# Performance work log

Hardware: AMD Instinct MI355X
Metric: run time of the kernel (lower is better)

## Reference

```python
import jax, jax.numpy as jnp
import numpy as np

B, N, D, H = 2, 2048, 256, 4
DH = D // H  # 64
ALPHA_DIV = 0.01
LN_EPS = 1e-5


def _split_heads(t):
    # [B, N, D] -> [B, H, N, DH]
    b, n, _ = t.shape
    return t.reshape(b, n, H, DH).transpose(0, 2, 1, 3)


def _merge_heads(t):
    # [B, H, N, DH] -> [B, N, D]
    b, h, n, d = t.shape
    return t.transpose(0, 2, 1, 3).reshape(b, n, h * d)


def setup_inputs() -> dict:
    key = jax.random.key(0)
    ks = jax.random.split(key, 20)
    p = lambda k, shape: (jax.random.normal(k, shape, dtype=jnp.float32) * 0.02)
    return {
        "x0": jax.random.normal(ks[0], (B, N, D), dtype=jnp.float32),
        "x1": jax.random.normal(ks[1], (B, N, D), dtype=jnp.float32),
        "cross_mask0": jax.random.uniform(ks[2], (B, 1, N), dtype=jnp.float32),
        "cross_mask1": jax.random.uniform(ks[3], (B, 1, N), dtype=jnp.float32),
        # weights stored as [in, out]
        "Wqk": p(ks[4], (D, D)), "bqk": jnp.zeros((D,), jnp.float32),
        "Wv": p(ks[5], (D, D)), "bv": jnp.zeros((D,), jnp.float32),
        "Wo": p(ks[6], (D, D)), "bo": jnp.zeros((D,), jnp.float32),
        "W1": p(ks[7], (2 * D, 2 * D)), "b1": jnp.zeros((2 * D,), jnp.float32),
        "ln_g": jnp.ones((2 * D,), jnp.float32), "ln_b": jnp.zeros((2 * D,), jnp.float32),
        "W2": p(ks[8], (2 * D, D)), "b2": jnp.zeros((D,), jnp.float32),
    }


def _ffn(x, W1, b1, ln_g, ln_b, W2, b2):
    h = x @ W1 + b1
    mu = jnp.mean(h, -1, keepdims=True)
    var = jnp.var(h, -1, keepdims=True)
    h = (h - mu) * jax.lax.rsqrt(var + LN_EPS) * ln_g + ln_b
    h = jax.nn.gelu(h, approximate=False)
    return h @ W2 + b2


def cross_block(x0, x1, cross_mask0, cross_mask1, Wqk, bqk, Wv, bv, Wo, bo,
                W1, b1, ln_g, ln_b, W2, b2):
    s = (DH ** -0.5) ** 0.5  # scale applied to each of qk0, qk1
    qk0 = _split_heads(x0 @ Wqk + bqk) * s
    qk1 = _split_heads(x1 @ Wqk + bqk) * s
    v0 = _split_heads(x0 @ Wv + bv)
    v1 = _split_heads(x1 @ Wv + bv)

    sim = jnp.einsum('bhid,bhjd->bhij', qk0, qk1)  # [B,H,N0,N1]

    # cross masks: [B,1,N] -> broadcast [B,1,1,N] over heads and query rows
    bad0 = (cross_mask0[:, :, None, :] < ALPHA_DIV)  # masks keys of dir 1->0
    bad1 = (cross_mask1[:, :, None, :] < ALPHA_DIV)  # masks keys of dir 0->1

    attn01 = jax.nn.softmax(jnp.where(bad1, -jnp.inf, sim), axis=-1)             # [B,H,N0,N1]
    attn10 = jax.nn.softmax(jnp.where(bad0, -jnp.inf, sim.swapaxes(-2, -1)), axis=-1)  # [B,H,N1,N0]

    m0 = jnp.einsum('bhij,bhjd->bhid', attn01, v1)
    m1 = jnp.einsum('bhij,bhjd->bhid', attn10, v0)

    m0 = _merge_heads(m0) @ Wo + bo
    m1 = _merge_heads(m1) @ Wo + bo

    out0 = x0 + _ffn(jnp.concatenate([x0, m0], -1), W1, b1, ln_g, ln_b, W2, b2)
    out1 = x1 + _ffn(jnp.concatenate([x1, m1], -1), W1, b1, ln_g, ln_b, W2, b2)
    return out0, out1, attn01, attn10


def reference(x0, x1, cross_mask0, cross_mask1, Wqk, bqk, Wv, bv, Wo, bo,
              W1, b1, ln_g, ln_b, W2, b2):
    return cross_block(x0, x1, cross_mask0, cross_mask1, Wqk, bqk, Wv, bv,
                       Wo, bo, W1, b1, ln_g, ln_b, W2, b2)
```

## Files before the change

kernel.cpp:

```cpp
#include <hip/hip_runtime.h>
#include <hip/hip_bf16.h>
#include <math.h>

#define B 2
#define N 2048
#define D 256
#define H 4
#define DH 64
#define D2 512
#define BH 8
#define BKP 40

static constexpr float ALPHA_DIV = 0.01f;
static constexpr float LN_EPS = 1e-5f;
static constexpr float SCL = 0.35355339059327373f;

typedef __attribute__((ext_vector_type(4))) float f32x4;
typedef __attribute__((ext_vector_type(8))) short s16x8;

template<int BM, bool OUT_BF16, bool HAS_RES>
__device__ __forceinline__ void gemm_core(
    __hip_bfloat16 (*As)[BKP], __hip_bfloat16 (*Ws)[BKP],
    const __hip_bfloat16* A, int lda, const __hip_bfloat16* WT, int ldw,
    const float* bias, const float* Res, int ldres,
    void* Cvp, int ldc, int K, float alpha, int rowBase, int colBase)
{
    constexpr int WM = BM / 2;
    constexpr int FM = WM / 16;
    constexpr int ACHUNK = (BM * 32) / (256 * 8);

    const int tid = threadIdx.x;
    const int lane = tid & 63, wid = tid >> 6;
    const int wr = wid >> 1, wc = wid & 1;
    const int lr = lane & 15, lk = (lane >> 4) * 8;

    f32x4 acc[FM][2] = {};

    for (int k0 = 0; k0 < K; k0 += 32) {
#pragma unroll
        for (int c = 0; c < ACHUNK; c++) {
            int e = (tid + c * 256) * 8;
            int r = e >> 5, kk = e & 31;
            *(s16x8*)&As[r][kk] = *(const s16x8*)&A[(size_t)(rowBase + r) * lda + k0 + kk];
        }
        {
            int e = tid * 8;
            int n = e >> 5, kk = e & 31;
            *(s16x8*)&Ws[n][kk] = *(const s16x8*)&WT[(size_t)(colBase + n) * ldw + k0 + kk];
        }
        __syncthreads();

        s16x8 a[FM], b[2];
#pragma unroll
        for (int i = 0; i < FM; i++) a[i] = *(const s16x8*)&As[wr * WM + i * 16 + lr][lk];
#pragma unroll
        for (int j = 0; j < 2; j++) b[j] = *(const s16x8*)&Ws[wc * 32 + j * 16 + lr][lk];
#pragma unroll
        for (int i = 0; i < FM; i++)
#pragma unroll
            for (int j = 0; j < 2; j++)
                acc[i][j] = __builtin_amdgcn_mfma_f32_16x16x32_bf16(a[i], b[j], acc[i][j], 0, 0, 0);
        __syncthreads();
    }

#pragma unroll
    for (int i = 0; i < FM; i++) {
#pragma unroll
        for (int j = 0; j < 2; j++) {
            int col = colBase + wc * 32 + j * 16 + lr;
            float bval = bias ? bias[col] : 0.f;
#pragma unroll
            for (int t = 0; t < 4; t++) {
                int row = rowBase + wr * WM + i * 16 + (lane >> 4) * 4 + t;
                float o = alpha * (acc[i][j][t] + bval);
                if (HAS_RES) o += Res[(size_t)row * ldres + col];
                if (OUT_BF16)
                    ((__hip_bfloat16*)Cvp)[(size_t)row * ldc + col] = __float2bfloat16(o);
                else
                    ((float*)Cvp)[(size_t)row * ldc + col] = o;
            }
        }
    }
}

template<bool OUT_BF16, bool HAS_RES>
__global__ __launch_bounds__(256) void gemm128_z(
    const __hip_bfloat16* A0, const __hip_bfloat16* A1, int lda,
    const __hip_bfloat16* WT, int ldw, const float* bias,
    const float* Res0, const float* Res1, int ldres,
    void* C0, void* C1, int ldc, int K, float alpha)
{
    __shared__ __hip_bfloat16 As[128][BKP];
    __shared__ __hip_bfloat16 Ws[64][BKP];
    const __hip_bfloat16* A = blockIdx.z ? A1 : A0;
    const float* Res = blockIdx.z ? Res1 : Res0;
    void* C = blockIdx.z ? C1 : C0;
    gemm_core<128, OUT_BF16, HAS_RES>(As, Ws, A, lda, WT, ldw, bias, Res, ldres,
        C, ldc, K, alpha, blockIdx.y * 128, blockIdx.x * 64);
}

__global__ __launch_bounds__(256) void proj_kernel(
    const float* __restrict__ x0, const float* __restrict__ x1,
    const __hip_bfloat16* __restrict__ WcT, const float* __restrict__ cb,
    __hip_bfloat16* __restrict__ qkv0, __hip_bfloat16* __restrict__ qkv1,
    __hip_bfloat16* __restrict__ vT,
    __hip_bfloat16* __restrict__ xc0, __hip_bfloat16* __restrict__ xc1)
{
    __shared__ __hip_bfloat16 As[128][BKP];
    __shared__ __hip_bfloat16 Ws[64][BKP];
    __shared__ __hip_bfloat16 T[128][72];
    const int z = blockIdx.z;
    const float* x = z ? x1 : x0;
    __hip_bfloat16* qkv = z ? qkv1 : qkv0;
    __hip_bfloat16* xc = z ? xc1 : xc0;
    const int rowBase = blockIdx.y * 128;
    const int colBase = blockIdx.x * 64;
    const int tid = threadIdx.x;
    const int lane = tid & 63, wid = tid >> 6;
    const int wr = wid >> 1, wc = wid & 1;
    const int lr = lane & 15, g = lane >> 4, lk = g * 8;

    f32x4 acc[4][2] = {};
    for (int k0 = 0; k0 < D; k0 += 32) {
#pragma unroll
        for (int c = 0; c < 2; c++) {
            int e = (tid + c * 256) * 8;
            int r = e >> 5, kk = e & 31;
            const float4 v0 = *(const float4*)&x[(size_t)(rowBase + r) * D + k0 + kk];
            const float4 v1 = *(const float4*)&x[(size_t)(rowBase + r) * D + k0 + kk + 4];
            union { s16x8 v; __hip_bfloat16 hh[8]; } u;
            u.hh[0] = __float2bfloat16(v0.x); u.hh[1] = __float2bfloat16(v0.y);
            u.hh[2] = __float2bfloat16(v0.z); u.hh[3] = __float2bfloat16(v0.w);
            u.hh[4] = __float2bfloat16(v1.x); u.hh[5] = __float2bfloat16(v1.y);
            u.hh[6] = __float2bfloat16(v1.z); u.hh[7] = __float2bfloat16(v1.w);
            *(s16x8*)&As[r][kk] = u.v;
            if (colBase == 0)
                *(s16x8*)&xc[(size_t)(rowBase + r) * D2 + k0 + kk] = u.v;
        }
        {
            int e = tid * 8;
            int n = e >> 5, kk = e & 31;
            *(s16x8*)&Ws[n][kk] = *(const s16x8*)&WcT[(size_t)(colBase + n) * D + k0 + kk];
        }
        __syncthreads();
        s16x8 a[4], b[2];
#pragma unroll
        for (int i = 0; i < 4; i++) a[i] = *(const s16x8*)&As[wr * 64 + i * 16 + lr][lk];
#pragma unroll
        for (int j = 0; j < 2; j++) b[j] = *(const s16x8*)&Ws[wc * 32 + j * 16 + lr][lk];
#pragma unroll
        for (int i = 0; i < 4; i++)
#pragma unroll
            for (int j = 0; j < 2; j++)
                acc[i][j] = __builtin_amdgcn_mfma_f32_16x16x32_bf16(a[i], b[j], acc[i][j], 0, 0, 0);
        __syncthreads();
    }

    if (colBase < 256) {
#pragma unroll
        for (int i = 0; i < 4; i++)
#pragma unroll
            for (int j = 0; j < 2; j++) {
                int col = colBase + wc * 32 + j * 16 + lr;
                float bval = cb[col];
#pragma unroll
                for (int t = 0; t < 4; t++) {
                    int row = rowBase + wr * 64 + i * 16 + g * 4 + t;
                    qkv[(size_t)row * D2 + col] = __float2bfloat16(acc[i][j][t] + bval);
                }
            }
    } else {
#pragma unroll
        for (int i = 0; i < 4; i++)
#pragma unroll
            for (int j = 0; j < 2; j++) {
                int cl = wc * 32 + j * 16 + lr;
                float bval = cb[colBase + cl];
#pragma unroll
                for (int t = 0; t < 4; t++)
                    T[wr * 64 + i * 16 + g * 4 + t][cl] = __float2bfloat16(acc[i][j][t] + bval);
            }
        __syncthreads();
        int hh = (colBase - 256) >> 6;
        int b_ = rowBase >> 11, n0 = rowBase & (N - 1);
        int slot = (z ? 0 : 8) + b_ * H + hh;
        int dh = tid >> 2, nn0 = (tid & 3) * 32;
        alignas(16) __hip_bfloat16 tmp[32];
#pragma unroll
        for (int u = 0; u < 32; u++) tmp[u] = T[nn0 + u][dh];
        __hip_bfloat16* dst = vT + ((size_t)slot * DH + dh) * N + n0 + nn0;
#pragma unroll
        for (int u8 = 0; u8 < 4; u8++)
            *(s16x8*)&dst[u8 * 8] = *(s16x8*)&tmp[u8 * 8];
    }
}

__device__ void transpose_tile(const float* W, int ldw, __hip_bfloat16* WT, int ldt,
                               int n0, int k0, float scale)
{
    __shared__ float T[32][33];
    int t = threadIdx.x;
    int r = t >> 3, c = (t & 7) * 4;
    float4 v = *(const float4*)&W[(size_t)(k0 + r) * ldw + n0 + c];
    T[r][c] = v.x; T[r][c + 1] = v.y; T[r][c + 2] = v.z; T[r][c + 3] = v.w;
    __syncthreads();
    __hip_bfloat16* dst = &WT[(size_t)(n0 + r) * ldt + k0 + c];
    dst[0] = __float2bfloat16(T[c][r] * scale);
    dst[1] = __float2bfloat16(T[c + 1][r] * scale);
    dst[2] = __float2bfloat16(T[c + 2][r] * scale);
    dst[3] = __float2bfloat16(T[c + 3][r] * scale);
}

__global__ __launch_bounds__(256) void prep_weights(
    const float* Wqk, const float* Wv, const float* W1, const float* W2,
    const float* bqk, const float* bv,
    __hip_bfloat16* WcT, __hip_bfloat16* W1cT, __hip_bfloat16* W2T,
    float* cb)
{
    int blk = blockIdx.x;
    if (blk < 64) {
        int nT = blk & 7, kT = blk >> 3;
        transpose_tile(Wqk, 256, WcT, 256, nT * 32, kT * 32, SCL);
    } else if (blk < 128) {
        int t = blk - 64; int nT = t & 7, kT = t >> 3;
        transpose_tile(Wv, 256, WcT + 256 * 256, 256, nT * 32, kT * 32, 1.f);
    } else if (blk < 256) {
        int t = blk - 128; int nT = t & 15, kT = t >> 4;
        transpose_tile(W1, 512, W1cT, 512, nT * 32, kT * 32, 1.f);
    } else if (blk < 384) {
        int t = blk - 256; int nT = t & 7, kT = t >> 3;
        transpose_tile(W2, 256, W2T, 512, nT * 32, kT * 32, 1.f);
    } else {
        int t = threadIdx.x;
        cb[t] = SCL * bqk[t];
        cb[256 + t] = bv[t];
    }
}

__global__ __launch_bounds__(256) void fuse_w(
    const float* __restrict__ Wo, const float* __restrict__ W1,
    const float* __restrict__ b1, const float* __restrict__ bo,
    __hip_bfloat16* __restrict__ W1cT, float* __restrict__ cb2)
{
    int blk = blockIdx.x;
    if (blk < 32) {
        __shared__ float As[64][17];
        __shared__ float Bs[64][17];
        int n0 = (blk & 7) * 64, k0 = (blk >> 3) * 64;
        int tx = threadIdx.x & 15, ty = threadIdx.x >> 4;
        float acc[4][4] = {};
        for (int c0 = 0; c0 < 256; c0 += 16) {
#pragma unroll
            for (int it = 0; it < 4; it++) {
                int idx = threadIdx.x + it * 256;
                int n = idx & 63, c = idx >> 6;
                As[n][c] = W1[(size_t)(256 + c0 + c) * 512 + n0 + n];
            }
#pragma unroll
            for (int it = 0; it < 4; it++) {
                int idx = threadIdx.x + it * 256;
                int k = idx >> 4, c = idx & 15;
                Bs[k][c] = Wo[(size_t)(k0 + k) * 256 + c0 + c];
            }
            __syncthreads();
#pragma unroll
            for (int c = 0; c < 16; c++) {
                float av[4], bv[4];
#pragma unroll
                for (int i = 0; i < 4; i++) av[i] = As[ty + i * 16][c];
#pragma unroll
                for (int j = 0; j < 4; j++) bv[j] = Bs[tx + j * 16][c];
#pragma unroll
                for (int i = 0; i < 4; i++)
#pragma unroll
                    for (int j = 0; j < 4; j++) acc[i][j] += av[i] * bv[j];
            }
            __syncthreads();
        }
#pragma unroll
        for (int i = 0; i < 4; i++)
#pragma unroll
            for (int j = 0; j < 4; j++)
                W1cT[(size_t)(n0 + ty + i * 16) * 512 + 256 + k0 + tx + j * 16] =
                    __float2bfloat16(acc[i][j]);
    } else {
        int n = (blk - 32) * 256 + threadIdx.x;
        float s = b1[n];
        for (int c = 0; c < 256; c++) s += bo[c] * W1[(size_t)(256 + c) * 512 + n];
        cb2[n] = s;
    }
}

__global__ __launch_bounds__(256) void fused_attn_av(
    const __hip_bfloat16* __restrict__ qkv0, const __hip_bfloat16* __restrict__ qkv1,
    const float* __restrict__ cm0, const float* __restrict__ cm1,
    const __hip_bfloat16* __restrict__ vT,
    float* __restrict__ attn01, float* __restrict__ attn10,
    __hip_bfloat16* __restrict__ xc0, __hip_bfloat16* __restrict__ xc1)
{
    __shared__ __hip_bfloat16 Kt[128][72];
    __shared__ __hip_bfloat16 Pfb[64][136];
    __shared__ float okm[2048];

    const int tid = threadIdx.x;
    int l = blockIdx.x;
    int xcd = l & 7, idx = l >> 3;
    int zz = xcd * 2 + (idx >> 5);
    int xb = idx & 31;
    int dir = zz >> 3, bh = zz & 7;
    int b = bh >> 2, h = bh & 3;

    const __hip_bfloat16* qQ = (dir ? qkv1 : qkv0) + (size_t)b * N * D2 + h * DH;
    const __hip_bfloat16* qK = (dir ? qkv0 : qkv1) + (size_t)b * N * D2 + h * DH;
    const float* cmK = (dir ? cm0 : cm1) + b * N;
    const __hip_bfloat16* vslot = vT + (size_t)((dir ? 8 : 0) + bh) * DH * N;
    float* attnOut = (dir ? attn10 : attn01) + (size_t)bh * N * N;
    __hip_bfloat16* mOut = (dir ? xc1 : xc0) + (size_t)b * N * D2 + 256 + h * DH;

    const int i0 = xb * 64;
    const int lane = tid & 63, w = tid >> 6;
    const int lr = lane & 15, g = lane >> 4;

    s16x8 a0 = *(const s16x8*)&qQ[(size_t)(i0 + w * 16 + lr) * D2 + g * 8];
    s16x8 a1 = *(const s16x8*)&qQ[(size_t)(i0 + w * 16 + lr) * D2 + 32 + g * 8];

#pragma unroll
    for (int it = 0; it < 8; it++) okm[tid + it * 256] = cmK[tid + it * 256];

    s16x8 kreg[4];
    auto loadK = [&](int jt) {
        const int kk0 = jt * 128;
#pragma unroll
        for (int c = 0; c < 4; c++) {
            int e = (tid + c * 256) * 8;
            kreg[c] = *(const s16x8*)&qK[(size_t)(kk0 + (e >> 6)) * D2 + (e & 63)];
        }
    };
    auto writeK = [&]() {
#pragma unroll
        for (int c = 0; c < 4; c++) {
            int e = (tid + c * 256) * 8;
            *(s16x8*)&Kt[e >> 6][e & 63] = kreg[c];
        }
    };

    float sp[4] = { 0.f, 0.f, 0.f, 0.f };
    loadK(0);
    for (int jt = 0; jt < 16; jt++) {
        writeK();
        __syncthreads();
        if (jt < 15) loadK(jt + 1);

        f32x4 accs[8] = {};
#pragma unroll
        for (int j = 0; j < 8; j++) {
            s16x8 bb = *(const s16x8*)&Kt[j * 16 + lr][g * 8];
            accs[j] = __builtin_amdgcn_mfma_f32_16x16x32_bf16(a0, bb, accs[j], 0, 0, 0);
        }
#pragma unroll
        for (int j = 0; j < 8; j++) {
            s16x8 bb = *(const s16x8*)&Kt[j * 16 + lr][32 + g * 8];
            accs[j] = __builtin_amdgcn_mfma_f32_16x16x32_bf16(a1, bb, accs[j], 0, 0, 0);
        }
        const int k0 = jt * 128;
#pragma unroll
        for (int j = 0; j < 8; j++) {
            bool ok = okm[k0 + j * 16 + lr] >= ALPHA_DIV;
#pragma unroll
            for (int t = 0; t < 4; t++)
                if (ok) sp[t] += __expf(accs[j][t]);
        }
        __syncthreads();
    }
    float inv[4];
#pragma unroll
    for (int t = 0; t < 4; t++) {
#pragma unroll
        for (int off = 1; off <= 8; off <<= 1) sp[t] += __shfl_xor(sp[t], off);
        inv[t] = 1.f / sp[t];
    }

    f32x4 acc_o[4] = {};
    loadK(0);
    for (int jt = 0; jt < 16; jt++) {
        writeK();
        __syncthreads();
        if (jt < 15) loadK(jt + 1);
        const int k0 = jt * 128;

        s16x8 vf[4][4];
#pragma unroll
        for (int ks = 0; ks < 4; ks++)
#pragma unroll
            for (int j = 0; j < 4; j++)
                vf[ks][j] = *(const s16x8*)&vslot[(size_t)(j * 16 + lr) * N + k0 + ks * 32 + g * 8];

        f32x4 accs[8] = {};
#pragma unroll
        for (int j = 0; j < 8; j++) {
            s16x8 bb = *(const s16x8*)&Kt[j * 16 + lr][g * 8];
            accs[j] = __builtin_amdgcn_mfma_f32_16x16x32_bf16(a0, bb, accs[j], 0, 0, 0);
        }
#pragma unroll
        for (int j = 0; j < 8; j++) {
            s16x8 bb = *(const s16x8*)&Kt[j * 16 + lr][32 + g * 8];
            accs[j] = __builtin_amdgcn_mfma_f32_16x16x32_bf16(a1, bb, accs[j], 0, 0, 0);
        }

#pragma unroll
        for (int j = 0; j < 8; j++) {
            bool ok = okm[k0 + j * 16 + lr] >= ALPHA_DIV;
#pragma unroll
            for (int t = 0; t < 4; t++) {
                float pv = ok ? __expf(accs[j][t]) * inv[t] : 0.f;
                Pfb[w * 16 + g * 4 + t][j * 16 + lr] = __float2bfloat16(pv);
            }
        }
        __syncthreads();

#pragma unroll
        for (int k = 0; k < 4; k++) {
            int f = tid + k * 256;
            int r = f >> 4, c0 = (f & 15) * 8;
            union { s16x8 v; __hip_bfloat16 hh[8]; } u;
            u.v = *(const s16x8*)&Pfb[r][c0];
            float4 o0, o1;
            o0.x = __bfloat162float(u.hh[0]); o0.y = __bfloat162float(u.hh[1]);
            o0.z = __bfloat162float(u.hh[2]); o0.w = __bfloat162float(u.hh[3]);
            o1.x = __bfloat162float(u.hh[4]); o1.y = __bfloat162float(u.hh[5]);
            o1.z = __bfloat162float(u.hh[6]); o1.w = __bfloat162float(u.hh[7]);
            *(float4*)&attnOut[(size_t)(i0 + r) * N + k0 + c0] = o0;
            *(float4*)&attnOut[(size_t)(i0 + r) * N + k0 + c0 + 4] = o1;
        }

#pragma unroll
        for (int ks = 0; ks < 4; ks++) {
            s16x8 pa = *(const s16x8*)&Pfb[w * 16 + lr][ks * 32 + g * 8];
#pragma unroll
            for (int j = 0; j < 4; j++)
                acc_o[j] = __builtin_amdgcn_mfma_f32_16x16x32_bf16(pa, vf[ks][j], acc_o[j], 0, 0, 0);
        }
        __syncthreads();
    }

    __hip_bfloat16* Ob = (__hip_bfloat16*)Pfb;
#pragma unroll
    for (int j = 0; j < 4; j++)
#pragma unroll
        for (int t = 0; t < 4; t++)
            Ob[(w * 16 + g * 4 + t) * 136 + j * 16 + lr] = __float2bfloat16(acc_o[j][t]);
    __syncthreads();
    {
        int row = tid >> 2, c0 = (tid & 3) * 16;
        *(s16x8*)&mOut[(size_t)(i0 + row) * D2 + c0]     = *(const s16x8*)&Ob[row * 136 + c0];
        *(s16x8*)&mOut[(size_t)(i0 + row) * D2 + c0 + 8] = *(const s16x8*)&Ob[row * 136 + c0 + 8];
    }
}

#define HS_LD 528
__global__ __launch_bounds__(256) void w1_ln_gelu(
    __hip_bfloat16* __restrict__ xc0, __hip_bfloat16* __restrict__ xc1,
    const __hip_bfloat16* __restrict__ W1T, const float* __restrict__ b1,
    const float* __restrict__ lng, const float* __restrict__ lnb)
{
    __shared__ __hip_bfloat16 As[32][BKP];
    __shared__ __hip_bfloat16 WH[512 * BKP];
    __shared__ float redS[4][32], redQ[4][32];

    __hip_bfloat16* xc = blockIdx.y ? xc1 : xc0;
    const int rowBase = blockIdx.x * 32;
    const int tid = threadIdx.x;
    const int w = tid >> 6, lane = tid & 63;
    const int lr = lane & 15, g = lane >> 4, lk = g * 8;

    f32x4 acc[2][8] = {};
    for (int k0 = 0; k0 < D2; k0 += 32) {
        if (tid < 128) {
            int e = tid * 8;
            int r = e >> 5, kk = e & 31;
            *(s16x8*)&As[r][kk] = *(const s16x8*)&xc[(size_t)(rowBase + r) * D2 + k0 + kk];
        }
#pragma unroll
        for (int c = 0; c < 8; c++) {
            int e = (tid + c * 256) * 8;
            int n = e >> 5, kk = e & 31;
            *(s16x8*)&WH[n * BKP + kk] = *(const s16x8*)&W1T[(size_t)n * D2 + k0 + kk];
        }
        __syncthreads();
        s16x8 a[2], b[8];
#pragma unroll
        for (int i = 0; i < 2; i++) a[i] = *(const s16x8*)&As[i * 16 + lr][lk];
#pragma unroll
        for (int j = 0; j < 8; j++) b[j] = *(const s16x8*)&WH[(w * 128 + j * 16 + lr) * BKP + lk];
#pragma unroll
        for (int i = 0; i < 2; i++)
#pragma unroll
            for (int j = 0; j < 8; j++)
                acc[i][j] = __builtin_amdgcn_mfma_f32_16x16x32_bf16(a[i], b[j], acc[i][j], 0, 0, 0);
        __syncthreads();
    }

    float cols_b[8];
#pragma unroll
    for (int j = 0; j < 8; j++) cols_b[j] = b1[w * 128 + j * 16 + lr];
#pragma unroll
    for (int i = 0; i < 2; i++) {
#pragma unroll
        for (int t = 0; t < 4; t++) {
            float s = 0.f, q = 0.f;
#pragma unroll
            for (int j = 0; j < 8; j++) {
                float hv = acc[i][j][t] + cols_b[j];
                acc[i][j][t] = hv;
                s += hv; q += hv * hv;
            }
#pragma unroll
            for (int off = 1; off <= 8; off <<= 1) {
                s += __shfl_xor(s, off);
                q += __shfl_xor(q, off);
            }
            if (lr == 0) {
                int row = i * 16 + g * 4 + t;
                redS[w][row] = s; redQ[w][row] = q;
            }
        }
    }
    __syncthreads();

    __hip_bfloat16* Hs = WH;
    float gcol[8], bcol[8];
#pragma unroll
    for (int j = 0; j < 8; j++) {
        gcol[j] = lng[w * 128 + j * 16 + lr];
        bcol[j] = lnb[w * 128 + j * 16 + lr];
    }
#pragma unroll
    for (int i = 0; i < 2; i++) {
#pragma unroll
        for (int t = 0; t < 4; t++) {
            int row = i * 16 + g * 4 + t;
            float sum = redS[0][row] + redS[1][row] + redS[2][row] + redS[3][row];
            float sq  = redQ[0][row] + redQ[1][row] + redQ[2][row] + redQ[3][row];
            float mu = sum * (1.f / 512.f);
            float var = sq * (1.f / 512.f) - mu * mu;
            float rstd = rsqrtf(var + LN_EPS);
#pragma unroll
            for (int j = 0; j < 8; j++) {
                float y = (acc[i][j][t] - mu) * rstd * gcol[j] + bcol[j];
                float ge = 0.5f * y * (1.f + erff(y * 0.70710678118654752f));
                Hs[row * HS_LD + w * 128 + j * 16 + lr] = __float2bfloat16(ge);
            }
        }
    }
    __syncthreads();

    {
        int row = tid >> 3, c0 = (tid & 7) * 64;
#pragma unroll
        for (int u = 0; u < 8; u++)
            *(s16x8*)&xc[(size_t)(rowBase + row) * D2 + c0 + u * 8] =
                *(s16x8*)&Hs[row * HS_LD + c0 + u * 8];
    }
}

extern "C" void kernel_launch(void* const* d_in, const int* in_sizes, int n_in,
                              void* d_out, int out_size, void* d_ws, size_t ws_size,
                              hipStream_t stream) {
    const float* x0  = (const float*)d_in[0];
    const float* x1  = (const float*)d_in[1];
    const float* cm0 = (const float*)d_in[2];
    const float* cm1 = (const float*)d_in[3];
    const float* Wqk = (const float*)d_in[4]; const float* bqk = (const float*)d_in[5];
    const float* Wv  = (const float*)d_in[6]; const float* bv  = (const float*)d_in[7];
    const float* Wo  = (const float*)d_in[8]; const float* bo  = (const float*)d_in[9];
    const float* W1  = (const float*)d_in[10]; const float* b1 = (const float*)d_in[11];
    const float* lng = (const float*)d_in[12]; const float* lnb = (const float*)d_in[13];
    const float* W2  = (const float*)d_in[14]; const float* b2 = (const float*)d_in[15];

    float* out = (float*)d_out;
    char* p = (char*)d_ws;

    const size_t XSZ = (size_t)B * N * D;
    auto alloc = [&](size_t bytes) { char* r = p; p += (bytes + 255) & ~255ull; return r; };
    __hip_bfloat16* qkv0 = (__hip_bfloat16*)alloc((size_t)B * N * D2 * 2);
    __hip_bfloat16* qkv1 = (__hip_bfloat16*)alloc((size_t)B * N * D2 * 2);
    __hip_bfloat16* vT   = (__hip_bfloat16*)alloc((size_t)16 * DH * N * 2);
    __hip_bfloat16* xc0  = (__hip_bfloat16*)alloc((size_t)B * N * D2 * 2);
    __hip_bfloat16* xc1  = (__hip_bfloat16*)alloc((size_t)B * N * D2 * 2);
    __hip_bfloat16* WcT  = (__hip_bfloat16*)alloc(512 * 256 * 2);
    __hip_bfloat16* W1cT = (__hip_bfloat16*)alloc(512 * 512 * 2);
    __hip_bfloat16* W2T  = (__hip_bfloat16*)alloc(256 * 512 * 2);
    float* cb            = (float*)alloc(512 * 4);
    float* cb2           = (float*)alloc(512 * 4);

    float* out0 = out;
    float* out1 = out + XSZ;
    float* attn01 = out + 2 * XSZ;
    float* attn10 = attn01 + (size_t)BH * N * N;

    dim3 blk(256);

    prep_weights<<<385, blk, 0, stream>>>(Wqk, Wv, W1, W2, bqk, bv,
                                          WcT, W1cT, W2T, cb);
    fuse_w<<<34, blk, 0, stream>>>(Wo, W1, b1, bo, W1cT, cb2);

    proj_kernel<<<dim3(8, 32, 2), blk, 0, stream>>>(
        x0, x1, WcT, cb, qkv0, qkv1, vT, xc0, xc1);

    fused_attn_av<<<512, blk, 0, stream>>>(qkv0, qkv1, cm0, cm1, vT,
        attn01, attn10, xc0, xc1);

    w1_ln_gelu<<<dim3(128, 2), blk, 0, stream>>>(xc0, xc1, W1cT, cb2, lng, lnb);

    gemm128_z<false, true><<<dim3(4, 32, 2), blk, 0, stream>>>(
        xc0, xc1, D2, W2T, D2, b2, x0, x1, D, out0, out1, D, D2, 1.f);
}
```

Measured before the change: 205.0 us.

## Halve query tile and split key columns across wave pairs in attention kernel

The fused attention kernel now processes 32 query rows per block instead of 64, launching 1024 blocks. Within a block, pairs of waves split each 128-key tile into two 64-column halves, reducing softmax denominators and partial PV outputs through shared memory. It also drops one barrier per tile, loads V fragments inline instead of prefetching into registers, and adds occupancy launch bounds. The aim is more parallelism and occupancy across CUs, at the cost of reloading K tiles twice as often overall and extra reduction overhead.

```diff
diff --git a/kernel.cpp b/kernel.cpp
--- a/kernel.cpp
+++ b/kernel.cpp
@@ -291,7 +291,7 @@
     }
 }
 
-__global__ __launch_bounds__(256) void fused_attn_av(
+__global__ __launch_bounds__(256, 4) void fused_attn_av(
     const __hip_bfloat16* __restrict__ qkv0, const __hip_bfloat16* __restrict__ qkv1,
     const float* __restrict__ cm0, const float* __restrict__ cm1,
     const __hip_bfloat16* __restrict__ vT,
@@ -299,14 +299,15 @@
     __hip_bfloat16* __restrict__ xc0, __hip_bfloat16* __restrict__ xc1)
 {
     __shared__ __hip_bfloat16 Kt[128][72];
-    __shared__ __hip_bfloat16 Pfb[64][136];
+    __shared__ __hip_bfloat16 Pfb[32][144];
     __shared__ float okm[2048];
+    __shared__ float redS[4][16];
 
     const int tid = threadIdx.x;
     int l = blockIdx.x;
     int xcd = l & 7, idx = l >> 3;
-    int zz = xcd * 2 + (idx >> 5);
-    int xb = idx & 31;
+    int zz = xcd * 2 + (idx >> 6);
+    int xb = idx & 63;
     int dir = zz >> 3, bh = zz & 7;
     int b = bh >> 2, h = bh & 3;
 
@@ -317,12 +318,14 @@
     float* attnOut = (dir ? attn10 : attn01) + (size_t)bh * N * N;
     __hip_bfloat16* mOut = (dir ? xc1 : xc0) + (size_t)b * N * D2 + 256 + h * DH;
 
-    const int i0 = xb * 64;
+    const int i0 = xb * 32;
     const int lane = tid & 63, w = tid >> 6;
+    const int f = w >> 1, hf = w & 1;
+    const int kb = hf * 64;
     const int lr = lane & 15, g = lane >> 4;
 
-    s16x8 a0 = *(const s16x8*)&qQ[(size_t)(i0 + w * 16 + lr) * D2 + g * 8];
-    s16x8 a1 = *(const s16x8*)&qQ[(size_t)(i0 + w * 16 + lr) * D2 + 32 + g * 8];
+    s16x8 a0 = *(const s16x8*)&qQ[(size_t)(i0 + f * 16 + lr) * D2 + g * 8];
+    s16x8 a1 = *(const s16x8*)&qQ[(size_t)(i0 + f * 16 + lr) * D2 + 32 + g * 8];
 
 #pragma unroll
     for (int it = 0; it < 8; it++) okm[tid + it * 256] = cmK[tid + it * 256];
@@ -351,34 +354,41 @@
         __syncthreads();
         if (jt < 15) loadK(jt + 1);
 
-        f32x4 accs[8] = {};
-#pragma unroll
-        for (int j = 0; j < 8; j++) {
-            s16x8 bb = *(const s16x8*)&Kt[j * 16 + lr][g * 8];
+        f32x4 accs[4] = {};
+#pragma unroll
+        for (int j = 0; j < 4; j++) {
+            s16x8 bb = *(const s16x8*)&Kt[kb + j * 16 + lr][g * 8];
             accs[j] = __builtin_amdgcn_mfma_f32_16x16x32_bf16(a0, bb, accs[j], 0, 0, 0);
         }
 #pragma unroll
-        for (int j = 0; j < 8; j++) {
-            s16x8 bb = *(const s16x8*)&Kt[j * 16 + lr][32 + g * 8];
+        for (int j = 0; j < 4; j++) {
+            s16x8 bb = *(const s16x8*)&Kt[kb + j * 16 + lr][32 + g * 8];
             accs[j] = __builtin_amdgcn_mfma_f32_16x16x32_bf16(a1, bb, accs[j], 0, 0, 0);
         }
         const int k0 = jt * 128;
 #pragma unroll
-        for (int j = 0; j < 8; j++) {
-            bool ok = okm[k0 + j * 16 + lr] >= ALPHA_DIV;
+        for (int j = 0; j < 4; j++) {
+            bool ok = okm[k0 + kb + j * 16 + lr] >= ALPHA_DIV;
 #pragma unroll
             for (int t = 0; t < 4; t++)
                 if (ok) sp[t] += __expf(accs[j][t]);
         }
         __syncthreads();
     }
+#pragma unroll
+    for (int t = 0; t < 4; t++) {
+#pragma unroll
+        for (int off = 1; off <= 8; off <<= 1) sp[t] += __shfl_xor(sp[t], off);
+    }
+    if (lr == 0) {
+#pragma unroll
+        for (int t = 0; t < 4; t++) redS[w][g * 4 + t] = sp[t];
+    }
+    __syncthreads();
     float inv[4];
 #pragma unroll
-    for (int t = 0; t < 4; t++) {
-#pragma unroll
-        for (int off = 1; off <= 8; off <<= 1) sp[t] += __shfl_xor(sp[t], off);
-        inv[t] = 1.f / sp[t];
-    }
+    for (int t = 0; t < 4; t++)
+        inv[t] = 1.f / (redS[f * 2][g * 4 + t] + redS[f * 2 + 1][g * 4 + t]);
 
     f32x4 acc_o[4] = {};
     loadK(0);
@@ -388,72 +398,79 @@
         if (jt < 15) loadK(jt + 1);
         const int k0 = jt * 128;
 
-        s16x8 vf[4][4];
-#pragma unroll
-        for (int ks = 0; ks < 4; ks++)
-#pragma unroll
-            for (int j = 0; j < 4; j++)
-                vf[ks][j] = *(const s16x8*)&vslot[(size_t)(j * 16 + lr) * N + k0 + ks * 32 + g * 8];
-
-        f32x4 accs[8] = {};
-#pragma unroll
-        for (int j = 0; j < 8; j++) {
-            s16x8 bb = *(const s16x8*)&Kt[j * 16 + lr][g * 8];
+        f32x4 accs[4] = {};
+#pragma unroll
+        for (int j = 0; j < 4; j++) {
+            s16x8 bb = *(const s16x8*)&Kt[kb + j * 16 + lr][g * 8];
             accs[j] = __builtin_amdgcn_mfma_f32_16x16x32_bf16(a0, bb, accs[j], 0, 0, 0);
         }
 #pragma unroll
-        for (int j = 0; j < 8; j++) {
-            s16x8 bb = *(const s16x8*)&Kt[j * 16 + lr][32 + g * 8];
+        for (int j = 0; j < 4; j++) {
+            s16x8 bb = *(const s16x8*)&Kt[kb + j * 16 + lr][32 + g * 8];
             accs[j] = __builtin_amdgcn_mfma_f32_16x16x32_bf16(a1, bb, accs[j], 0, 0, 0);
         }
 
 #pragma unroll
-        for (int j = 0; j < 8; j++) {
-            bool ok = okm[k0 + j * 16 + lr] >= ALPHA_DIV;
+        for (int j = 0; j < 4; j++) {
+            bool ok = okm[k0 + kb + j * 16 + lr] >= ALPHA_DIV;
 #pragma unroll
             for (int t = 0; t < 4; t++) {
                 float pv = ok ? __expf(accs[j][t]) * inv[t] : 0.f;
-                Pfb[w * 16 + g * 4 + t][j * 16 + lr] = __float2bfloat16(pv);
-            }
-        }
-        __syncthreads();
-
-#pragma unroll
-        for (int k = 0; k < 4; k++) {
-            int f = tid + k * 256;
-            int r = f >> 4, c0 = (f & 15) * 8;
+                Pfb[f * 16 + g * 4 + t][kb + j * 16 + lr] = __float2bfloat16(pv);
+            }
+        }
+
+        {
+            int r = f * 16 + (lane >> 2), cs = kb + (lane & 3) * 16;
             union { s16x8 v; __hip_bfloat16 hh[8]; } u;
-            u.v = *(const s16x8*)&Pfb[r][c0];
-            float4 o0, o1;
-            o0.x = __bfloat162float(u.hh[0]); o0.y = __bfloat162float(u.hh[1]);
-            o0.z = __bfloat162float(u.hh[2]); o0.w = __bfloat162float(u.hh[3]);
-            o1.x = __bfloat162float(u.hh[4]); o1.y = __bfloat162float(u.hh[5]);
-            o1.z = __bfloat162float(u.hh[6]); o1.w = __bfloat162float(u.hh[7]);
-            *(float4*)&attnOut[(size_t)(i0 + r) * N + k0 + c0] = o0;
-            *(float4*)&attnOut[(size_t)(i0 + r) * N + k0 + c0 + 4] = o1;
-        }
-
-#pragma unroll
-        for (int ks = 0; ks < 4; ks++) {
-            s16x8 pa = *(const s16x8*)&Pfb[w * 16 + lr][ks * 32 + g * 8];
-#pragma unroll
-            for (int j = 0; j < 4; j++)
-                acc_o[j] = __builtin_amdgcn_mfma_f32_16x16x32_bf16(pa, vf[ks][j], acc_o[j], 0, 0, 0);
-        }
-        __syncthreads();
-    }
-
-    __hip_bfloat16* Ob = (__hip_bfloat16*)Pfb;
-#pragma unroll
-    for (int j = 0; j < 4; j++)
-#pragma unroll
-        for (int t = 0; t < 4; t++)
-            Ob[(w * 16 + g * 4 + t) * 136 + j * 16 + lr] = __float2bfloat16(acc_o[j][t]);
+#pragma unroll
+            for (int half = 0; half < 2; half++) {
+                u.v = *(const s16x8*)&Pfb[r][cs + half * 8];
+                float4 o;
+                o.x = __bfloat162float(u.hh[0]); o.y = __bfloat162float(u.hh[1]);
+                o.z = __bfloat162float(u.hh[2]); o.w = __bfloat162float(u.hh[3]);
+                *(float4*)&attnOut[(size_t)(i0 + r) * N + k0 + cs + half * 8] = o;
+                o.x = __bfloat162float(u.hh[4]); o.y = __bfloat162float(u.hh[5]);
+                o.z = __bfloat162float(u.hh[6]); o.w = __bfloat162float(u.hh[7]);
+                *(float4*)&attnOut[(size_t)(i0 + r) * N + k0 + cs + half * 8 + 4] = o;
+            }
+        }
+
+#pragma unroll
+        for (int ks = 0; ks < 2; ks++) {
+            s16x8 pa = *(const s16x8*)&Pfb[f * 16 + lr][kb + ks * 32 + g * 8];
+#pragma unroll
+            for (int j = 0; j < 4; j++) {
+                s16x8 vb = *(const s16x8*)&vslot[(size_t)(j * 16 + lr) * N + k0 + kb + ks * 32 + g * 8];
+                acc_o[j] = __builtin_amdgcn_mfma_f32_16x16x32_bf16(pa, vb, acc_o[j], 0, 0, 0);
+            }
+        }
+        __syncthreads();
+    }
+
+    float (*Of)[72] = (float(*)[72])Pfb;
+    if (hf == 0) {
+#pragma unroll
+        for (int j = 0; j < 4; j++)
+#pragma unroll
+            for (int t = 0; t < 4; t++)
+                Of[f * 16 + g * 4 + t][j * 16 + lr] = acc_o[j][t];
+    }
+    __syncthreads();
+    if (hf == 1) {
+#pragma unroll
+        for (int j = 0; j < 4; j++)
+#pragma unroll
+            for (int t = 0; t < 4; t++)
+                Of[f * 16 + g * 4 + t][j * 16 + lr] += acc_o[j][t];
+    }
     __syncthreads();
     {
-        int row = tid >> 2, c0 = (tid & 3) * 16;
-        *(s16x8*)&mOut[(size_t)(i0 + row) * D2 + c0]     = *(const s16x8*)&Ob[row * 136 + c0];
-        *(s16x8*)&mOut[(size_t)(i0 + row) * D2 + c0 + 8] = *(const s16x8*)&Ob[row * 136 + c0 + 8];
+        int row = tid >> 3, c0 = (tid & 7) * 8;
+        union { s16x8 v; __hip_bfloat16 hh[8]; } u;
+#pragma unroll
+        for (int i = 0; i < 8; i++) u.hh[i] = __float2bfloat16(Of[row][c0 + i]);
+        *(s16x8*)&mOut[(size_t)(i0 + row) * D2 + c0] = u.v;
     }
 }
 
@@ -607,7 +624,7 @@
     proj_kernel<<<dim3(8, 32, 2), blk, 0, stream>>>(
         x0, x1, WcT, cb, qkv0, qkv1, vT, xc0, xc1);
 
-    fused_attn_av<<<512, blk, 0, stream>>>(qkv0, qkv1, cm0, cm1, vT,
+    fused_attn_av<<<1024, blk, 0, stream>>>(qkv0, qkv1, cm0, cm1, vT,
         attn01, attn10, xc0, xc1);
 
     w1_ln_gelu<<<dim3(128, 2), blk, 0, stream>>>(xc0, xc1, W1cT, cb2, lng, lnb);
```

Result: slower. 228.2 us (+11.3%).

## Fuse W2 GEMM into the LN/GELU kernel and merge weight-prep launches

Applied to the files above, without the earlier changes.

The second FFN GEMM, with its bias and residual add, now runs at the end of the W1+LayerNorm+GELU kernel, straight from the GELU activations held in shared memory. This drops the bf16 write-back of the hidden activations, their re-read and one kernel launch. The Wo·W1 weight-folding kernel is also merged into prep_weights as extra blocks, removing another launch. In the fused tail each wave reads W2T fragments directly from global memory without staging them in shared memory, which may add L2 traffic.

```diff
diff --git a/kernel.cpp b/kernel.cpp
--- a/kernel.cpp
+++ b/kernel.cpp
@@ -17,87 +17,6 @@
 
 typedef __attribute__((ext_vector_type(4))) float f32x4;
 typedef __attribute__((ext_vector_type(8))) short s16x8;
-
-template<int BM, bool OUT_BF16, bool HAS_RES>
-__device__ __forceinline__ void gemm_core(
-    __hip_bfloat16 (*As)[BKP], __hip_bfloat16 (*Ws)[BKP],
-    const __hip_bfloat16* A, int lda, const __hip_bfloat16* WT, int ldw,
-    const float* bias, const float* Res, int ldres,
-    void* Cvp, int ldc, int K, float alpha, int rowBase, int colBase)
-{
-    constexpr int WM = BM / 2;
-    constexpr int FM = WM / 16;
-    constexpr int ACHUNK = (BM * 32) / (256 * 8);
-
-    const int tid = threadIdx.x;
-    const int lane = tid & 63, wid = tid >> 6;
-    const int wr = wid >> 1, wc = wid & 1;
-    const int lr = lane & 15, lk = (lane >> 4) * 8;
-
-    f32x4 acc[FM][2] = {};
-
-    for (int k0 = 0; k0 < K; k0 += 32) {
-#pragma unroll
-        for (int c = 0; c < ACHUNK; c++) {
-            int e = (tid + c * 256) * 8;
-            int r = e >> 5, kk = e & 31;
-            *(s16x8*)&As[r][kk] = *(const s16x8*)&A[(size_t)(rowBase + r) * lda + k0 + kk];
-        }
-        {
-            int e = tid * 8;
-            int n = e >> 5, kk = e & 31;
-            *(s16x8*)&Ws[n][kk] = *(const s16x8*)&WT[(size_t)(colBase + n) * ldw + k0 + kk];
-        }
-        __syncthreads();
-
-        s16x8 a[FM], b[2];
-#pragma unroll
-        for (int i = 0; i < FM; i++) a[i] = *(const s16x8*)&As[wr * WM + i * 16 + lr][lk];
-#pragma unroll
-        for (int j = 0; j < 2; j++) b[j] = *(const s16x8*)&Ws[wc * 32 + j * 16 + lr][lk];
-#pragma unroll
-        for (int i = 0; i < FM; i++)
-#pragma unroll
-            for (int j = 0; j < 2; j++)
-                acc[i][j] = __builtin_amdgcn_mfma_f32_16x16x32_bf16(a[i], b[j], acc[i][j], 0, 0, 0);
-        __syncthreads();
-    }
-
-#pragma unroll
-    for (int i = 0; i < FM; i++) {
-#pragma unroll
-        for (int j = 0; j < 2; j++) {
-            int col = colBase + wc * 32 + j * 16 + lr;
-            float bval = bias ? bias[col] : 0.f;
-#pragma unroll
-            for (int t = 0; t < 4; t++) {
-                int row = rowBase + wr * WM + i * 16 + (lane >> 4) * 4 + t;
-                float o = alpha * (acc[i][j][t] + bval);
-                if (HAS_RES) o += Res[(size_t)row * ldres + col];
-                if (OUT_BF16)
-                    ((__hip_bfloat16*)Cvp)[(size_t)row * ldc + col] = __float2bfloat16(o);
-                else
-                    ((float*)Cvp)[(size_t)row * ldc + col] = o;
-            }
-        }
-    }
-}
-
-template<bool OUT_BF16, bool HAS_RES>
-__global__ __launch_bounds__(256) void gemm128_z(
-    const __hip_bfloat16* A0, const __hip_bfloat16* A1, int lda,
-    const __hip_bfloat16* WT, int ldw, const float* bias,
-    const float* Res0, const float* Res1, int ldres,
-    void* C0, void* C1, int ldc, int K, float alpha)
-{
-    __shared__ __hip_bfloat16 As[128][BKP];
-    __shared__ __hip_bfloat16 Ws[64][BKP];
-    const __hip_bfloat16* A = blockIdx.z ? A1 : A0;
-    const float* Res = blockIdx.z ? Res1 : Res0;
-    void* C = blockIdx.z ? C1 : C0;
-    gemm_core<128, OUT_BF16, HAS_RES>(As, Ws, A, lda, WT, ldw, bias, Res, ldres,
-        C, ldc, K, alpha, blockIdx.y * 128, blockIdx.x * 64);
-}
 
 __global__ __launch_bounds__(256) void proj_kernel(
     const float* __restrict__ x0, const float* __restrict__ x1,
@@ -212,10 +131,11 @@
 }
 
 __global__ __launch_bounds__(256) void prep_weights(
-    const float* Wqk, const float* Wv, const float* W1, const float* W2,
-    const float* bqk, const float* bv,
+    const float* Wqk, const float* Wv, const float* Wo,
+    const float* W1, const float* W2,
+    const float* bqk, const float* bv, const float* b1, const float* bo,
     __hip_bfloat16* WcT, __hip_bfloat16* W1cT, __hip_bfloat16* W2T,
-    float* cb)
+    float* cb, float* cb2)
 {
     int blk = blockIdx.x;
     if (blk < 64) {
@@ -230,64 +150,56 @@
     } else if (blk < 384) {
         int t = blk - 256; int nT = t & 7, kT = t >> 3;
         transpose_tile(W2, 256, W2T, 512, nT * 32, kT * 32, 1.f);
+    } else if (blk < 416) {
+        __shared__ float As[64][17];
+        __shared__ float Bs[64][17];
+        int t2 = blk - 384;
+        int n0 = (t2 & 7) * 64, k0 = (t2 >> 3) * 64;
+        int tx = threadIdx.x & 15, ty = threadIdx.x >> 4;
+        float acc[4][4] = {};
+        for (int c0 = 0; c0 < 256; c0 += 16) {
+#pragma unroll
+            for (int it = 0; it < 4; it++) {
+                int idx = threadIdx.x + it * 256;
+                int n = idx & 63, c = idx >> 6;
+                As[n][c] = W1[(size_t)(256 + c0 + c) * 512 + n0 + n];
+            }
+#pragma unroll
+            for (int it = 0; it < 4; it++) {
+                int idx = threadIdx.x + it * 256;
+                int k = idx >> 4, c = idx & 15;
+                Bs[k][c] = Wo[(size_t)(k0 + k) * 256 + c0 + c];
+            }
+            __syncthreads();
+#pragma unroll
+            for (int c = 0; c < 16; c++) {
+                float av[4], bv2[4];
+#pragma unroll
+                for (int i = 0; i < 4; i++) av[i] = As[ty + i * 16][c];
+#pragma unroll
+                for (int j = 0; j < 4; j++) bv2[j] = Bs[tx + j * 16][c];
+#pragma unroll
+                for (int i = 0; i < 4; i++)
+#pragma unroll
+                    for (int j = 0; j < 4; j++) acc[i][j] += av[i] * bv2[j];
+            }
+            __syncthreads();
+        }
+#pragma unroll
+        for (int i = 0; i < 4; i++)
+#pragma unroll
+            for (int j = 0; j < 4; j++)
+                W1cT[(size_t)(n0 + ty + i * 16) * 512 + 256 + k0 + tx + j * 16] =
+                    __float2bfloat16(acc[i][j]);
+    } else if (blk < 418) {
+        int n = (blk - 416) * 256 + threadIdx.x;
+        float s = b1[n];
+        for (int c = 0; c < 256; c++) s += bo[c] * W1[(size_t)(256 + c) * 512 + n];
+        cb2[n] = s;
     } else {
         int t = threadIdx.x;
         cb[t] = SCL * bqk[t];
         cb[256 + t] = bv[t];
-    }
-}
-
-__global__ __launch_bounds__(256) void fuse_w(
-    const float* __restrict__ Wo, const float* __restrict__ W1,
-    const float* __restrict__ b1, const float* __restrict__ bo,
-    __hip_bfloat16* __restrict__ W1cT, float* __restrict__ cb2)
-{
-    int blk = blockIdx.x;
-    if (blk < 32) {
-        __shared__ float As[64][17];
-        __shared__ float Bs[64][17];
-        int n0 = (blk & 7) * 64, k0 = (blk >> 3) * 64;
-        int tx = threadIdx.x & 15, ty = threadIdx.x >> 4;
-        float acc[4][4] = {};
-        for (int c0 = 0; c0 < 256; c0 += 16) {
-#pragma unroll
-            for (int it = 0; it < 4; it++) {
-                int idx = threadIdx.x + it * 256;
-                int n = idx & 63, c = idx >> 6;
-                As[n][c] = W1[(size_t)(256 + c0 + c) * 512 + n0 + n];
-            }
-#pragma unroll
-            for (int it = 0; it < 4; it++) {
-                int idx = threadIdx.x + it * 256;
-                int k = idx >> 4, c = idx & 15;
-                Bs[k][c] = Wo[(size_t)(k0 + k) * 256 + c0 + c];
-            }
-            __syncthreads();
-#pragma unroll
-            for (int c = 0; c < 16; c++) {
-                float av[4], bv[4];
-#pragma unroll
-                for (int i = 0; i < 4; i++) av[i] = As[ty + i * 16][c];
-#pragma unroll
-                for (int j = 0; j < 4; j++) bv[j] = Bs[tx + j * 16][c];
-#pragma unroll
-                for (int i = 0; i < 4; i++)
-#pragma unroll
-                    for (int j = 0; j < 4; j++) acc[i][j] += av[i] * bv[j];
-            }
-            __syncthreads();
-        }
-#pragma unroll
-        for (int i = 0; i < 4; i++)
-#pragma unroll
-            for (int j = 0; j < 4; j++)
-                W1cT[(size_t)(n0 + ty + i * 16) * 512 + 256 + k0 + tx + j * 16] =
-                    __float2bfloat16(acc[i][j]);
-    } else {
-        int n = (blk - 32) * 256 + threadIdx.x;
-        float s = b1[n];
-        for (int c = 0; c < 256; c++) s += bo[c] * W1[(size_t)(256 + c) * 512 + n];
-        cb2[n] = s;
     }
 }
 
@@ -458,16 +370,21 @@
 }
 
 #define HS_LD 528
-__global__ __launch_bounds__(256) void w1_ln_gelu(
-    __hip_bfloat16* __restrict__ xc0, __hip_bfloat16* __restrict__ xc1,
+__global__ __launch_bounds__(256) void ffn_tail(
+    const __hip_bfloat16* __restrict__ xc0, const __hip_bfloat16* __restrict__ xc1,
     const __hip_bfloat16* __restrict__ W1T, const float* __restrict__ b1,
-    const float* __restrict__ lng, const float* __restrict__ lnb)
+    const float* __restrict__ lng, const float* __restrict__ lnb,
+    const __hip_bfloat16* __restrict__ W2T, const float* __restrict__ b2,
+    const float* __restrict__ x0, const float* __restrict__ x1,
+    float* __restrict__ out0, float* __restrict__ out1)
 {
     __shared__ __hip_bfloat16 As[32][BKP];
     __shared__ __hip_bfloat16 WH[512 * BKP];
     __shared__ float redS[4][32], redQ[4][32];
 
-    __hip_bfloat16* xc = blockIdx.y ? xc1 : xc0;
+    const __hip_bfloat16* xc = blockIdx.y ? xc1 : xc0;
+    const float* xres = blockIdx.y ? x1 : x0;
+    float* outp = blockIdx.y ? out1 : out0;
     const int rowBase = blockIdx.x * 32;
     const int tid = threadIdx.x;
     const int w = tid >> 6, lane = tid & 63;
@@ -554,12 +471,34 @@
     }
     __syncthreads();
 
-    {
-        int row = tid >> 3, c0 = (tid & 7) * 64;
-#pragma unroll
-        for (int u = 0; u < 8; u++)
-            *(s16x8*)&xc[(size_t)(rowBase + row) * D2 + c0 + u * 8] =
-                *(s16x8*)&Hs[row * HS_LD + c0 + u * 8];
+    f32x4 acc2[2][4] = {};
+    for (int k0 = 0; k0 < D2; k0 += 32) {
+        s16x8 a[2], b[4];
+#pragma unroll
+        for (int i = 0; i < 2; i++)
+            a[i] = *(const s16x8*)&Hs[(i * 16 + lr) * HS_LD + k0 + lk];
+#pragma unroll
+        for (int j = 0; j < 4; j++)
+            b[j] = *(const s16x8*)&W2T[(size_t)(w * 64 + j * 16 + lr) * D2 + k0 + lk];
+#pragma unroll
+        for (int i = 0; i < 2; i++)
+#pragma unroll
+            for (int j = 0; j < 4; j++)
+                acc2[i][j] = __builtin_amdgcn_mfma_f32_16x16x32_bf16(a[i], b[j], acc2[i][j], 0, 0, 0);
+    }
+#pragma unroll
+    for (int i = 0; i < 2; i++) {
+#pragma unroll
+        for (int j = 0; j < 4; j++) {
+            int col = w * 64 + j * 16 + lr;
+            float bval = b2[col];
+#pragma unroll
+            for (int t = 0; t < 4; t++) {
+                int row = rowBase + i * 16 + g * 4 + t;
+                outp[(size_t)row * D + col] =
+                    acc2[i][j][t] + bval + xres[(size_t)row * D + col];
+            }
+        }
     }
 }
 
@@ -600,9 +539,8 @@
 
     dim3 blk(256);
 
-    prep_weights<<<385, blk, 0, stream>>>(Wqk, Wv, W1, W2, bqk, bv,
-                                          WcT, W1cT, W2T, cb);
-    fuse_w<<<34, blk, 0, stream>>>(Wo, W1, b1, bo, W1cT, cb2);
+    prep_weights<<<419, blk, 0, stream>>>(Wqk, Wv, Wo, W1, W2, bqk, bv, b1, bo,
+                                          WcT, W1cT, W2T, cb, cb2);
 
     proj_kernel<<<dim3(8, 32, 2), blk, 0, stream>>>(
         x0, x1, WcT, cb, qkv0, qkv1, vT, xc0, xc1);
@@ -610,8 +548,6 @@
     fused_attn_av<<<512, blk, 0, stream>>>(qkv0, qkv1, cm0, cm1, vT,
         attn01, attn10, xc0, xc1);
 
-    w1_ln_gelu<<<dim3(128, 2), blk, 0, stream>>>(xc0, xc1, W1cT, cb2, lng, lnb);
-
-    gemm128_z<false, true><<<dim3(4, 32, 2), blk, 0, stream>>>(
-        xc0, xc1, D2, W2T, D2, b2, x0, x1, D, out0, out1, D, D2, 1.f);
+    ffn_tail<<<dim3(128, 2), blk, 0, stream>>>(
+        xc0, xc1, W1cT, cb2, lng, lnb, W2T, b2, x0, x1, out0, out1);
 }
```

After: 189.0 us. -7.8%, faster.
